# Performance work log

Measured on AMD Instinct MI355X. Metric: run time of the kernel, lower is better.

Reference implementation:

```python
import jax, jax.numpy as jnp
import numpy as np

N_NODES = 50000
N_FEAT = 128
DIM = 10
N_EDGES = 1600000
N_GRAPHS = 1000


def setup_inputs() -> dict:
    key = jax.random.key(0)
    ks = jax.random.split(key, 8)
    x = jax.random.normal(ks[0], (N_NODES, N_FEAT), dtype=jnp.float32)
    W1_l = jax.random.normal(ks[1], (DIM, N_FEAT), dtype=jnp.float32) * 0.1
    W1_r = jax.random.normal(ks[2], (DIM, N_FEAT), dtype=jnp.float32) * 0.1
    W2_l = jax.random.normal(ks[3], (DIM, DIM), dtype=jnp.float32) * 0.3
    W2_r = jax.random.normal(ks[4], (DIM, DIM), dtype=jnp.float32) * 0.3
    Wfc = jax.random.normal(ks[5], (1, DIM), dtype=jnp.float32) * 0.3
    edge_index = jax.random.randint(ks[6], (2, N_EDGES), 0, N_NODES, dtype=jnp.int64)
    batch = jnp.sort(jax.random.randint(ks[7], (N_NODES,), 0, N_GRAPHS, dtype=jnp.int64))
    return {"x": x, "W1_l": W1_l, "W1_r": W1_r, "W2_l": W2_l, "W2_r": W2_r,
            "Wfc": Wfc, "edge_index": edge_index, "batch": batch}


def _sage_conv(h, src, dst, deg_inv, Wl, Wr):
    # mean aggregation over incoming neighbors, then two bias-free linears
    agg = jax.ops.segment_sum(h[src], dst, num_segments=N_NODES)  # [N, F]
    agg = agg * deg_inv[:, None]
    return agg @ Wl.T + h @ Wr.T


def reference(x, W1_l, W1_r, W2_l, W2_r, Wfc, edge_index, batch):
    src, dst = edge_index[0], edge_index[1]
    # in-degree per destination node (mean denominator, clamped at 1 like PyG)
    deg = jax.ops.segment_sum(jnp.ones((src.shape[0],), x.dtype), dst, num_segments=N_NODES)
    deg_inv = 1.0 / jnp.maximum(deg, 1.0)

    h = jax.nn.relu(_sage_conv(x, src, dst, deg_inv, W1_l, W1_r))
    h = _sage_conv(h, src, dst, deg_inv, W2_l, W2_r)

    # global mean pool over graphs
    counts = jax.ops.segment_sum(jnp.ones((N_NODES,), x.dtype), batch, num_segments=N_GRAPHS)
    pooled = jax.ops.segment_sum(h, batch, num_segments=N_GRAPHS)
    pooled = pooled / jnp.maximum(counts, 1.0)[:, None]

    return jax.nn.sigmoid(pooled @ Wfc.T)  # [N_GRAPHS, 1]
```

## Files before the change

kernel.cpp:

```cpp
#include <hip/hip_runtime.h>
#include <hip/hip_bf16.h>
#include <math.h>

#define N_NODES  50000
#define N_FEAT   128
#define DIM      10
#define N_EDGES  1600000
#define N_GRAPHS 1000
#define PSTRIDE  16
#define CAP      80
#define BSH      7
#define BNODES   128
#define NBUCK    391
#define BCAP     4608
#define ACHUNK   4096
#define ABLOCKS  ((N_EDGES + ACHUNK - 1) / ACHUNK)
#define PBLOCKS4 ((N_NODES * 4 + 255) / 256)
#define SPLIT    4
#define GSLOTS   128
#define SENT     50000


__device__ __forceinline__ float bf2f(unsigned short u) {
    union { unsigned int i; float f; } v;
    v.i = ((unsigned int)u) << 16;
    return v.f;
}

__device__ __forceinline__ float wload(const void* w, int fm, int i) {
    return fm ? ((const float*)w)[i] : bf2f(((const unsigned short*)w)[i]);
}

__device__ __forceinline__ int iload(const void* p, int im, long long pos) {
    return im ? (int)((const long long*)p)[pos] : ((const int*)p)[pos];
}

__global__ void detect_setup_kernel(
    const unsigned short* __restrict__ w1l, const unsigned int* __restrict__ ei32,
    const void* __restrict__ W2l, const void* __restrict__ W2r,
    const void* __restrict__ Wfc,
    int* __restrict__ fmode, int* __restrict__ imode,
    float* __restrict__ vl, float* __restrict__ vr,
    int* __restrict__ bcur, float* __restrict__ gsum, float* __restrict__ gcnt,
    float* __restrict__ p) {
    __shared__ int bigcnt, oddnz;
    if (threadIdx.x == 0) { bigcnt = 0; oddnz = 0; }
    __syncthreads();
    for (int i = threadIdx.x; i < DIM * N_FEAT; i += 256) {
        int expo = (w1l[i] >> 7) & 0xFF;
        if (expo >= 0x90) atomicAdd(&bigcnt, 1);
    }
    for (int i = threadIdx.x; i < 2048; i += 256) {
        if (ei32[2 * i + 1] != 0) atomicAdd(&oddnz, 1);
    }
    for (int i = threadIdx.x; i < NBUCK; i += 256) bcur[i] = 0;
    for (int i = threadIdx.x; i < N_GRAPHS; i += 256) { gsum[i] = 0.f; gcnt[i] = 0.f; }
    if (threadIdx.x < PSTRIDE) p[(size_t)SENT * PSTRIDE + threadIdx.x] = 0.f;
    __syncthreads();
    int fm = (bigcnt >= 4) ? 1 : 0;
    if (threadIdx.x == 0) { *fmode = fm; *imode = (oddnz == 0) ? 1 : 0; }
    int j = threadIdx.x;
    if (j < DIM) {
        float al = 0.f, ar = 0.f;
        for (int i = 0; i < DIM; i++) {
            float w = wload(Wfc, fm, i);
            al += w * wload(W2l, fm, i * DIM + j);
            ar += w * wload(W2r, fm, i * DIM + j);
        }
        vl[j] = al;
        vr[j] = ar;
    } else if (j < 16) {
        vl[j] = 0.f;
        vr[j] = 0.f;
    }
}

#define ACCUM8(f0)                                                  \
    _Pragma("unroll")                                               \
    for (int d = 0; d < DIM; d++) {                                 \
        _Pragma("unroll")                                           \
        for (int k = 0; k < 8; k++) {                               \
            accl[d] += xf[k] * wl[d * N_FEAT + (f0) + k];           \
            accr[d] += xf[k] * wr[d * N_FEAT + (f0) + k];           \
        }                                                           \
    }

__global__ __launch_bounds__(256) void fusedA_kernel(
    const void* __restrict__ ei, const void* __restrict__ x,
    const void* __restrict__ W1l, const void* __restrict__ W1r,
    const int* __restrict__ fmode, const int* __restrict__ imode,
    int* __restrict__ bcur, unsigned int* __restrict__ bedges,
    float* __restrict__ p, float* __restrict__ q) {
    __shared__ union U {
        struct { unsigned int stage[ACHUNK]; int hcnt[NBUCK]; int hbase[NBUCK]; } a;
        struct { float wl[DIM * N_FEAT]; float wr[DIM * N_FEAT]; } b;
    } sh;

    if (blockIdx.x < ABLOCKS) {
        int im = *imode;
        for (int b = threadIdx.x; b < NBUCK; b += 256) sh.a.hcnt[b] = 0;
        __syncthreads();
        long long e0 = (long long)blockIdx.x * ACHUNK;
        int nE = (int)min((long long)ACHUNK, (long long)N_EDGES - e0);
        for (int i = threadIdx.x; i < nE; i += 256) {
            int s = iload(ei, im, e0 + i);
            int d = iload(ei, im, (long long)N_EDGES + e0 + i);
            sh.a.stage[i] = (unsigned)s | ((unsigned)(d & (BNODES - 1)) << 16) | ((unsigned)(d >> BSH) << 23);
            atomicAdd(&sh.a.hcnt[d >> BSH], 1);
        }
        __syncthreads();
        for (int b = threadIdx.x; b < NBUCK; b += 256) {
            int c = sh.a.hcnt[b];
            sh.a.hbase[b] = c ? atomicAdd(&bcur[b], c) : 0;
            sh.a.hcnt[b] = 0;
        }
        __syncthreads();
        for (int i = threadIdx.x; i < nE; i += 256) {
            unsigned rec = sh.a.stage[i];
            int b = rec >> 23;
            int pos = sh.a.hbase[b] + atomicAdd(&sh.a.hcnt[b], 1);
            if (pos < BCAP) bedges[(size_t)b * BCAP + pos] = rec;
        }
    } else {
        int fm = *fmode;
        float* wl = sh.b.wl;
        float* wr = sh.b.wr;
        for (int i = threadIdx.x; i < DIM * N_FEAT; i += 256) {
            wl[i] = wload(W1l, fm, i);
            wr[i] = wload(W1r, fm, i);
        }
        __syncthreads();
        int tid4 = (blockIdx.x - ABLOCKS) * 256 + threadIdx.x;
        int n = tid4 >> 2;
        int sub = tid4 & 3;
        if (n >= N_NODES) return;

        float accl[DIM], accr[DIM];
#pragma unroll
        for (int d = 0; d < DIM; d++) { accl[d] = 0.f; accr[d] = 0.f; }

        if (fm) {
            const float4* xr = reinterpret_cast<const float4*>((const float*)x + (size_t)n * N_FEAT);
#pragma unroll
            for (int j = 0; j < 4; j++) {
                int fb = j * 4 + sub;
                float4 v0 = xr[2 * fb];
                float4 v1 = xr[2 * fb + 1];
                float xf[8] = {v0.x, v0.y, v0.z, v0.w, v1.x, v1.y, v1.z, v1.w};
                ACCUM8(fb * 8)
            }
        } else {
            const uint4* xr = reinterpret_cast<const uint4*>((const unsigned short*)x + (size_t)n * N_FEAT);
#pragma unroll
            for (int j = 0; j < 4; j++) {
                int fb = j * 4 + sub;
                uint4 v = xr[fb];
                float xf[8];
                xf[0] = bf2f((unsigned short)(v.x & 0xffff)); xf[1] = bf2f((unsigned short)(v.x >> 16));
                xf[2] = bf2f((unsigned short)(v.y & 0xffff)); xf[3] = bf2f((unsigned short)(v.y >> 16));
                xf[4] = bf2f((unsigned short)(v.z & 0xffff)); xf[5] = bf2f((unsigned short)(v.z >> 16));
                xf[6] = bf2f((unsigned short)(v.w & 0xffff)); xf[7] = bf2f((unsigned short)(v.w >> 16));
                ACCUM8(fb * 8)
            }
        }
#pragma unroll
        for (int d = 0; d < DIM; d++) {
            accl[d] += __shfl_xor(accl[d], 1, 4);
            accl[d] += __shfl_xor(accl[d], 2, 4);
            accr[d] += __shfl_xor(accr[d], 1, 4);
            accr[d] += __shfl_xor(accr[d], 2, 4);
        }
        if (sub == 0) {
            float4* pr = reinterpret_cast<float4*>(p + (size_t)n * PSTRIDE);
            float4* qr = reinterpret_cast<float4*>(q + (size_t)n * PSTRIDE);
            pr[0] = make_float4(accl[0], accl[1], accl[2], accl[3]);
            pr[1] = make_float4(accl[4], accl[5], accl[6], accl[7]);
            pr[2] = make_float4(accl[8], accl[9], 0.f, 0.f);
            pr[3] = make_float4(0.f, 0.f, 0.f, 0.f);
            qr[0] = make_float4(accr[0], accr[1], accr[2], accr[3]);
            qr[1] = make_float4(accr[4], accr[5], accr[6], accr[7]);
            qr[2] = make_float4(accr[8], accr[9], 0.f, 0.f);
            qr[3] = make_float4(0.f, 0.f, 0.f, 0.f);
        }
    }
}

__global__ __launch_bounds__(512) void pullB_kernel(
    const int* __restrict__ bcur, const unsigned int* __restrict__ bedges,
    const float* __restrict__ p, const float* __restrict__ q,
    const float* __restrict__ vl, const float* __restrict__ vr,
    float* __restrict__ t, float* __restrict__ u, float* __restrict__ dinv) {
    __shared__ unsigned short lcol[BNODES * CAP];
    __shared__ int lcnt[BNODES];
    const unsigned int s2 = (unsigned)SENT | ((unsigned)SENT << 16);
    uint4 sv = make_uint4(s2, s2, s2, s2);
    uint4* l4 = reinterpret_cast<uint4*>(lcol);
    for (int i = threadIdx.x; i < BNODES * CAP * 2 / 16; i += 512) l4[i] = sv;
    if (threadIdx.x < BNODES) lcnt[threadIdx.x] = 0;
    __syncthreads();

    int b = blockIdx.x;
    int m = min(bcur[b], BCAP);
    const unsigned int* seg = bedges + (size_t)b * BCAP;
    for (int i = threadIdx.x; i < m; i += 512) {
        unsigned rec = seg[i];
        int nidx = (rec >> 16) & (BNODES - 1);
        int pos = atomicAdd(&lcnt[nidx], 1);
        if (pos < CAP) lcol[nidx * CAP + pos] = (unsigned short)(rec & 0xffffu);
    }
    __syncthreads();

    int n = threadIdx.x >> 2;
    int sub4 = (threadIdx.x & 3) * 4;
    int g = (b << BSH) + n;
    if (g >= N_NODES) return;
    int deg = lcnt[n];
    int dcl = min(deg, CAP);
    const unsigned short* cl = lcol + n * CAP;
    float ax = 0.f, ay = 0.f, az = 0.f, aw = 0.f;
    for (int k0 = 0; k0 < dcl; k0 += 8) {
        uint4 cv = *reinterpret_cast<const uint4*>(cl + k0);
        unsigned c[8];
        c[0] = cv.x & 0xffff; c[1] = cv.x >> 16;
        c[2] = cv.y & 0xffff; c[3] = cv.y >> 16;
        c[4] = cv.z & 0xffff; c[5] = cv.z >> 16;
        c[6] = cv.w & 0xffff; c[7] = cv.w >> 16;
#pragma unroll
        for (int j = 0; j < 8; j++) {
            const float4 v = *reinterpret_cast<const float4*>(p + (size_t)c[j] * PSTRIDE + sub4);
            ax += v.x; ay += v.y; az += v.z; aw += v.w;
        }
    }
    float di = 1.0f / fmaxf((float)deg, 1.0f);
    float4 qv  = *reinterpret_cast<const float4*>(q + (size_t)g * PSTRIDE + sub4);
    float4 vlv = *reinterpret_cast<const float4*>(vl + sub4);
    float4 vrv = *reinterpret_cast<const float4*>(vr + sub4);
    float hx = fmaxf(ax * di + qv.x, 0.f);
    float hy = fmaxf(ay * di + qv.y, 0.f);
    float hz = fmaxf(az * di + qv.z, 0.f);
    float hw = fmaxf(aw * di + qv.w, 0.f);
    float tv = hx * vlv.x + hy * vlv.y + hz * vlv.z + hw * vlv.w;
    float uv = hx * vrv.x + hy * vrv.y + hz * vrv.z + hw * vrv.w;
    tv += __shfl_xor(tv, 1, 4); tv += __shfl_xor(tv, 2, 4);
    uv += __shfl_xor(uv, 1, 4); uv += __shfl_xor(uv, 2, 4);
    if ((threadIdx.x & 3) == 0) {
        t[g] = tv;
        u[g] = uv;
        dinv[g] = di;
    }
}

__global__ __launch_bounds__(256) void pull2B_kernel(
    const int* __restrict__ bcur, const unsigned int* __restrict__ bedges,
    const float* __restrict__ t, const float* __restrict__ u,
    const float* __restrict__ dinv, const void* __restrict__ batch,
    const int* __restrict__ imode,
    float* __restrict__ gsum, float* __restrict__ gcnt) {
    __shared__ float lnode[BNODES];
    __shared__ float ldinv[BNODES];
    __shared__ int   lb[BNODES];
    __shared__ float lgs[GSLOTS];
    __shared__ float lgc[GSLOTS];
    int b = blockIdx.x / SPLIT;
    int s = blockIdx.x % SPLIT;
    int tid = threadIdx.x;
    int node0 = b << BSH;
    int nvalid = min(BNODES, N_NODES - node0);
    int im = *imode;
    if (tid < BNODES) lnode[tid] = 0.f;
    if (tid < nvalid) {
        ldinv[tid] = dinv[node0 + tid];
        lb[tid] = iload(batch, im, node0 + tid);
    }
    if (tid < GSLOTS) { lgs[tid] = 0.f; lgc[tid] = 0.f; }
    __syncthreads();
    int m = min(bcur[b], BCAP);
    int c0 = (m * s) / SPLIT, c1 = (m * (s + 1)) / SPLIT;
    const unsigned int* seg = bedges + (size_t)b * BCAP;
    for (int i = c0 + tid; i < c1; i += 256) {
        unsigned rec = seg[i];
        int src  = rec & 0xffffu;
        int nidx = (rec >> 16) & (BNODES - 1);
        atomicAdd(&lnode[nidx], t[src]);
    }
    __syncthreads();
    int g0 = lb[0];
    int rng = lb[nvalid - 1] - g0 + 1;
    bool useLDS = (rng <= GSLOTS);
    if (tid < nvalid) {
        float gv = lnode[tid] * ldinv[tid];
        if (s == 0) gv += u[node0 + tid];
        int gg = lb[tid];
        if (useLDS) {
            atomicAdd(&lgs[gg - g0], gv);
            if (s == 0) atomicAdd(&lgc[gg - g0], 1.0f);
        } else {
            if (gv != 0.f) atomicAdd(gsum + gg, gv);
            if (s == 0) atomicAdd(gcnt + gg, 1.0f);
        }
    }
    __syncthreads();
    if (useLDS) {
        for (int i = tid; i < rng; i += 256) {
            float v = lgs[i];
            if (v != 0.f) atomicAdd(gsum + g0 + i, v);
            if (s == 0) {
                float c = lgc[i];
                if (c != 0.f) atomicAdd(gcnt + g0 + i, c);
            }
        }
    }
}

__global__ __launch_bounds__(256) void final_kernel(
    const float* __restrict__ gsum, const float* __restrict__ gcnt,
    const int* __restrict__ fmode, void* __restrict__ out) {
    int g = blockIdx.x * 256 + threadIdx.x;
    if (g >= N_GRAPHS) return;
    float pooled = gsum[g] / fmaxf(gcnt[g], 1.0f);
    float sg = 1.0f / (1.0f + expf(-pooled));
    if (*fmode) {
        ((float*)out)[g] = sg;
    } else {
        ((__hip_bfloat16*)out)[g] = __float2bfloat16(sg);
    }
}

extern "C" void kernel_launch(void* const* d_in, const int* in_sizes, int n_in,
                              void* d_out, int out_size, void* d_ws, size_t ws_size,
                              hipStream_t stream) {
    const void* x    = d_in[0];
    const void* W1l  = d_in[1];
    const void* W1r  = d_in[2];
    const void* W2l  = d_in[3];
    const void* W2r  = d_in[4];
    const void* Wfc  = d_in[5];
    const void* ei   = d_in[6];
    const void* batc = d_in[7];

    char* ws = (char*)d_ws;
    int*   fmode = (int*)ws;
    int*   imode = fmode + 1;
    float* vl   = (float*)(ws + 64);
    float* vr   = vl + 16;
    int*   bcur = (int*)(vr + 16);
    float* gsum = (float*)(bcur + NBUCK);
    float* gcnt = gsum + N_GRAPHS;
    unsigned int* bedges = (unsigned int*)(ws + ((((size_t)(gcnt + N_GRAPHS) - (size_t)ws) + 255) & ~(size_t)255));
    float* p    = (float*)(bedges + (size_t)NBUCK * BCAP);
    float* q    = p + (size_t)(N_NODES + 1) * PSTRIDE;
    float* t    = q + (size_t)N_NODES * PSTRIDE;
    float* u    = t + N_NODES;
    float* dinv = u + N_NODES;

    detect_setup_kernel<<<1, 256, 0, stream>>>(
        (const unsigned short*)W1l, (const unsigned int*)ei, W2l, W2r, Wfc,
        fmode, imode, vl, vr, bcur, gsum, gcnt, p);
    fusedA_kernel<<<ABLOCKS + PBLOCKS4, 256, 0, stream>>>(
        ei, x, W1l, W1r, fmode, imode, bcur, bedges, p, q);
    pullB_kernel<<<NBUCK, 512, 0, stream>>>(bcur, bedges, p, q, vl, vr, t, u, dinv);
    pull2B_kernel<<<NBUCK * SPLIT, 256, 0, stream>>>(bcur, bedges, t, u, dinv, batc, imode, gsum, gcnt);
    final_kernel<<<(N_GRAPHS + 255) / 256, 256, 0, stream>>>(gsum, gcnt, fmode, d_out);
}
```

Measured before the change: 154.5 us.

## Remove setup kernel by probing dtype inline and recompute vectors per block

Removes the single-block detect/setup kernel. Each kernel now probes the input dtypes inline from a few weight and edge words, buffers are zeroed with hipMemsetAsync, and pullB recomputes the folded W2·Wfc vectors in shared memory. The edge bucketing pass no longer stages records in LDS and instead re-reads the edge indices from global memory in the scatter pass, which cuts LDS use and may raise occupancy at the cost of a second global read. SPLIT drops from 4 to 2, and the probes now sample fewer elements, which makes dtype detection less robust.

```diff
diff --git a/kernel.cpp b/kernel.cpp
--- a/kernel.cpp
+++ b/kernel.cpp
@@ -16,7 +16,7 @@
 #define ACHUNK   4096
 #define ABLOCKS  ((N_EDGES + ACHUNK - 1) / ACHUNK)
 #define PBLOCKS4 ((N_NODES * 4 + 255) / 256)
-#define SPLIT    4
+#define SPLIT    2
 #define GSLOTS   128
 #define SENT     50000
 
@@ -32,47 +32,25 @@
 }
 
 __device__ __forceinline__ int iload(const void* p, int im, long long pos) {
-    return im ? (int)((const long long*)p)[pos] : ((const int*)p)[pos];
-}
-
-__global__ void detect_setup_kernel(
-    const unsigned short* __restrict__ w1l, const unsigned int* __restrict__ ei32,
-    const void* __restrict__ W2l, const void* __restrict__ W2r,
-    const void* __restrict__ Wfc,
-    int* __restrict__ fmode, int* __restrict__ imode,
-    float* __restrict__ vl, float* __restrict__ vr,
-    int* __restrict__ bcur, float* __restrict__ gsum, float* __restrict__ gcnt,
-    float* __restrict__ p) {
-    __shared__ int bigcnt, oddnz;
-    if (threadIdx.x == 0) { bigcnt = 0; oddnz = 0; }
-    __syncthreads();
-    for (int i = threadIdx.x; i < DIM * N_FEAT; i += 256) {
-        int expo = (w1l[i] >> 7) & 0xFF;
-        if (expo >= 0x90) atomicAdd(&bigcnt, 1);
-    }
-    for (int i = threadIdx.x; i < 2048; i += 256) {
-        if (ei32[2 * i + 1] != 0) atomicAdd(&oddnz, 1);
-    }
-    for (int i = threadIdx.x; i < NBUCK; i += 256) bcur[i] = 0;
-    for (int i = threadIdx.x; i < N_GRAPHS; i += 256) { gsum[i] = 0.f; gcnt[i] = 0.f; }
-    if (threadIdx.x < PSTRIDE) p[(size_t)SENT * PSTRIDE + threadIdx.x] = 0.f;
-    __syncthreads();
-    int fm = (bigcnt >= 4) ? 1 : 0;
-    if (threadIdx.x == 0) { *fmode = fm; *imode = (oddnz == 0) ? 1 : 0; }
-    int j = threadIdx.x;
-    if (j < DIM) {
-        float al = 0.f, ar = 0.f;
-        for (int i = 0; i < DIM; i++) {
-            float w = wload(Wfc, fm, i);
-            al += w * wload(W2l, fm, i * DIM + j);
-            ar += w * wload(W2r, fm, i * DIM + j);
-        }
-        vl[j] = al;
-        vr[j] = ar;
-    } else if (j < 16) {
-        vl[j] = 0.f;
-        vr[j] = 0.f;
-    }
+    return im ? ((const int*)p)[2 * pos] : ((const int*)p)[pos];
+}
+
+__device__ __forceinline__ int probe_fm(const void* W1l) {
+    const unsigned short* w = (const unsigned short*)W1l;
+    int hits = 0;
+#pragma unroll
+    for (int i = 0; i < 128; i++) {
+        int expo = (w[2 * i] >> 7) & 0xFF;
+        hits += (expo >= 0x90) ? 1 : 0;
+    }
+    return (hits >= 4) ? 1 : 0;
+}
+__device__ __forceinline__ int probe_im(const void* ei) {
+    const unsigned int* e = (const unsigned int*)ei;
+    unsigned o = 0;
+#pragma unroll
+    for (int i = 0; i < 8; i++) o |= e[2 * i + 1];
+    return (o == 0) ? 1 : 0;
 }
 
 #define ACCUM8(f0)                                                  \
@@ -88,24 +66,21 @@
 __global__ __launch_bounds__(256) void fusedA_kernel(
     const void* __restrict__ ei, const void* __restrict__ x,
     const void* __restrict__ W1l, const void* __restrict__ W1r,
-    const int* __restrict__ fmode, const int* __restrict__ imode,
     int* __restrict__ bcur, unsigned int* __restrict__ bedges,
     float* __restrict__ p, float* __restrict__ q) {
     __shared__ union U {
-        struct { unsigned int stage[ACHUNK]; int hcnt[NBUCK]; int hbase[NBUCK]; } a;
+        struct { int hcnt[NBUCK]; int hbase[NBUCK]; } a;
         struct { float wl[DIM * N_FEAT]; float wr[DIM * N_FEAT]; } b;
     } sh;
 
     if (blockIdx.x < ABLOCKS) {
-        int im = *imode;
+        int im = probe_im(ei);
         for (int b = threadIdx.x; b < NBUCK; b += 256) sh.a.hcnt[b] = 0;
         __syncthreads();
         long long e0 = (long long)blockIdx.x * ACHUNK;
         int nE = (int)min((long long)ACHUNK, (long long)N_EDGES - e0);
         for (int i = threadIdx.x; i < nE; i += 256) {
-            int s = iload(ei, im, e0 + i);
             int d = iload(ei, im, (long long)N_EDGES + e0 + i);
-            sh.a.stage[i] = (unsigned)s | ((unsigned)(d & (BNODES - 1)) << 16) | ((unsigned)(d >> BSH) << 23);
             atomicAdd(&sh.a.hcnt[d >> BSH], 1);
         }
         __syncthreads();
@@ -116,13 +91,17 @@
         }
         __syncthreads();
         for (int i = threadIdx.x; i < nE; i += 256) {
-            unsigned rec = sh.a.stage[i];
-            int b = rec >> 23;
+            int s = iload(ei, im, e0 + i);
+            int d = iload(ei, im, (long long)N_EDGES + e0 + i);
+            unsigned rec = (unsigned)s | ((unsigned)(d & (BNODES - 1)) << 16) | ((unsigned)(d >> BSH) << 23);
+            int b = d >> BSH;
             int pos = sh.a.hbase[b] + atomicAdd(&sh.a.hcnt[b], 1);
             if (pos < BCAP) bedges[(size_t)b * BCAP + pos] = rec;
         }
     } else {
-        int fm = *fmode;
+        int fm = probe_fm(W1l);
+        if (blockIdx.x == ABLOCKS && threadIdx.x < PSTRIDE)
+            p[(size_t)SENT * PSTRIDE + threadIdx.x] = 0.f;
         float* wl = sh.b.wl;
         float* wr = sh.b.wr;
         for (int i = threadIdx.x; i < DIM * N_FEAT; i += 256) {
@@ -188,10 +167,25 @@
 __global__ __launch_bounds__(512) void pullB_kernel(
     const int* __restrict__ bcur, const unsigned int* __restrict__ bedges,
     const float* __restrict__ p, const float* __restrict__ q,
-    const float* __restrict__ vl, const float* __restrict__ vr,
+    const void* __restrict__ W1l, const void* __restrict__ W2l,
+    const void* __restrict__ W2r, const void* __restrict__ Wfc,
     float* __restrict__ t, float* __restrict__ u, float* __restrict__ dinv) {
     __shared__ unsigned short lcol[BNODES * CAP];
     __shared__ int lcnt[BNODES];
+    __shared__ float svl[16], svr[16];
+    int fm = probe_fm(W1l);
+    if (threadIdx.x < 16) {
+        float al = 0.f, ar = 0.f;
+        if (threadIdx.x < DIM) {
+            for (int i = 0; i < DIM; i++) {
+                float w = wload(Wfc, fm, i);
+                al += w * wload(W2l, fm, i * DIM + threadIdx.x);
+                ar += w * wload(W2r, fm, i * DIM + threadIdx.x);
+            }
+        }
+        svl[threadIdx.x] = al;
+        svr[threadIdx.x] = ar;
+    }
     const unsigned int s2 = (unsigned)SENT | ((unsigned)SENT << 16);
     uint4 sv = make_uint4(s2, s2, s2, s2);
     uint4* l4 = reinterpret_cast<uint4*>(lcol);
@@ -233,8 +227,8 @@
     }
     float di = 1.0f / fmaxf((float)deg, 1.0f);
     float4 qv  = *reinterpret_cast<const float4*>(q + (size_t)g * PSTRIDE + sub4);
-    float4 vlv = *reinterpret_cast<const float4*>(vl + sub4);
-    float4 vrv = *reinterpret_cast<const float4*>(vr + sub4);
+    float4 vlv = *reinterpret_cast<const float4*>(svl + sub4);
+    float4 vrv = *reinterpret_cast<const float4*>(svr + sub4);
     float hx = fmaxf(ax * di + qv.x, 0.f);
     float hy = fmaxf(ay * di + qv.y, 0.f);
     float hz = fmaxf(az * di + qv.z, 0.f);
@@ -254,19 +248,19 @@
     const int* __restrict__ bcur, const unsigned int* __restrict__ bedges,
     const float* __restrict__ t, const float* __restrict__ u,
     const float* __restrict__ dinv, const void* __restrict__ batch,
-    const int* __restrict__ imode,
+    const void* __restrict__ ei,
     float* __restrict__ gsum, float* __restrict__ gcnt) {
     __shared__ float lnode[BNODES];
     __shared__ float ldinv[BNODES];
     __shared__ int   lb[BNODES];
     __shared__ float lgs[GSLOTS];
     __shared__ float lgc[GSLOTS];
+    int im = probe_im(ei);
     int b = blockIdx.x / SPLIT;
     int s = blockIdx.x % SPLIT;
     int tid = threadIdx.x;
     int node0 = b << BSH;
     int nvalid = min(BNODES, N_NODES - node0);
-    int im = *imode;
     if (tid < BNODES) lnode[tid] = 0.f;
     if (tid < nvalid) {
         ldinv[tid] = dinv[node0 + tid];
@@ -314,12 +308,13 @@
 
 __global__ __launch_bounds__(256) void final_kernel(
     const float* __restrict__ gsum, const float* __restrict__ gcnt,
-    const int* __restrict__ fmode, void* __restrict__ out) {
+    const void* __restrict__ W1l, void* __restrict__ out) {
+    int fm = probe_fm(W1l);
     int g = blockIdx.x * 256 + threadIdx.x;
     if (g >= N_GRAPHS) return;
     float pooled = gsum[g] / fmaxf(gcnt[g], 1.0f);
     float sg = 1.0f / (1.0f + expf(-pooled));
-    if (*fmode) {
+    if (fm) {
         ((float*)out)[g] = sg;
     } else {
         ((__hip_bfloat16*)out)[g] = __float2bfloat16(sg);
@@ -339,11 +334,7 @@
     const void* batc = d_in[7];
 
     char* ws = (char*)d_ws;
-    int*   fmode = (int*)ws;
-    int*   imode = fmode + 1;
-    float* vl   = (float*)(ws + 64);
-    float* vr   = vl + 16;
-    int*   bcur = (int*)(vr + 16);
+    int*   bcur = (int*)ws;
     float* gsum = (float*)(bcur + NBUCK);
     float* gcnt = gsum + N_GRAPHS;
     unsigned int* bedges = (unsigned int*)(ws + ((((size_t)(gcnt + N_GRAPHS) - (size_t)ws) + 255) & ~(size_t)255));
@@ -353,12 +344,11 @@
     float* u    = t + N_NODES;
     float* dinv = u + N_NODES;
 
-    detect_setup_kernel<<<1, 256, 0, stream>>>(
-        (const unsigned short*)W1l, (const unsigned int*)ei, W2l, W2r, Wfc,
-        fmode, imode, vl, vr, bcur, gsum, gcnt, p);
+    hipMemsetAsync(bcur, 0, (NBUCK + 2 * N_GRAPHS) * sizeof(int), stream);
     fusedA_kernel<<<ABLOCKS + PBLOCKS4, 256, 0, stream>>>(
-        ei, x, W1l, W1r, fmode, imode, bcur, bedges, p, q);
-    pullB_kernel<<<NBUCK, 512, 0, stream>>>(bcur, bedges, p, q, vl, vr, t, u, dinv);
-    pull2B_kernel<<<NBUCK * SPLIT, 256, 0, stream>>>(bcur, bedges, t, u, dinv, batc, imode, gsum, gcnt);
-    final_kernel<<<(N_GRAPHS + 255) / 256, 256, 0, stream>>>(gsum, gcnt, fmode, d_out);
-}
+        ei, x, W1l, W1r, bcur, bedges, p, q);
+    pullB_kernel<<<NBUCK, 512, 0, stream>>>(bcur, bedges, p, q,
+                                            W1l, W2l, W2r, Wfc, t, u, dinv);
+    pull2B_kernel<<<NBUCK * SPLIT, 256, 0, stream>>>(bcur, bedges, t, u, dinv, batc, ei, gsum, gcnt);
+    final_kernel<<<(N_GRAPHS + 255) / 256, 256, 0, stream>>>(gsum, gcnt, W1l, d_out);
+}
```

Result: slower. 163.9 us (+6.1%).
